# Kernel optimization log

Measured on AMD Instinct MI355X. Metric: run time of the kernel, lower is better.

Reference implementation:

```python
import jax, jax.numpy as jnp
import numpy as np

N, M, D, H, T = 8192, 8192, 64, 32, 8
KERNEL_SCALE = 1.0


def setup_inputs() -> dict:
    key = jax.random.key(0)
    ks = jax.random.split(key, 8)
    s1 = 1.0 / np.sqrt(D)
    s2 = 1.0 / np.sqrt(H)
    return {
        "X": jax.random.normal(ks[0], (N, D), jnp.float32),
        "Y": jax.random.normal(ks[1], (M, D), jnp.float32),
        "Y_target": jax.random.normal(ks[2], (M, T), jnp.float32),
        "W1": jax.random.normal(ks[3], (D, H), jnp.float32) * s1,
        "b1": jnp.zeros((H,), jnp.float32),
        "W2": jax.random.normal(ks[4], (H, H), jnp.float32) * s2,
        "b2": jnp.zeros((H,), jnp.float32),
        "W3": jax.random.normal(ks[5], (H, H), jnp.float32) * s2,
        "b3": jnp.zeros((H,), jnp.float32),
    }


def _mlp(x, W1, b1, W2, b2, W3, b3):
    h = jax.nn.relu(x @ W1 + b1)
    h = jax.nn.relu(h @ W2 + b2)
    return jax.nn.relu(h @ W3 + b3)


def reference(X, Y, Y_target, W1, b1, W2, b2, W3, b3):
    Xf = _mlp(X, W1, b1, W2, b2, W3, b3)  # [N, H]
    Yf = _mlp(Y, W1, b1, W2, b2, W3, b3)  # [M, H]
    sq = (
        jnp.sum(Xf * Xf, axis=1, keepdims=True)
        + jnp.sum(Yf * Yf, axis=1)[None, :]
        - 2.0 * (Xf @ Yf.T)
    )
    sq = jnp.maximum(sq, 0.0)  # guard tiny negatives from cancellation
    kernel = jnp.exp(-sq / (2.0 * KERNEL_SCALE**2))  # [N, M]
    weights = kernel / jnp.sum(kernel, axis=1, keepdims=True)
    return weights @ Y_target  # [N, T]
```

## Files before the change

kernel.cpp:

```cpp
#include <hip/hip_runtime.h>
#include <hip/hip_bf16.h>
#include <cstddef>

#define N_ROWS 8192
#define M_ROWS 8192
#define D_IN   64
#define H_DIM  32
#define T_OUT  8

#define NSPLIT   16
#define JSLICE   (M_ROWS / NSPLIT)
#define JTILE    32
#define NTILES   (JSLICE / JTILE)
#define LOG2E    1.4426950408889634f
#define NHALF_SC (-0.72134752044448169f)
#define PSTRIDE  34

typedef _Float16 half8  __attribute__((ext_vector_type(8)));
typedef __fp16   fp16x2 __attribute__((ext_vector_type(2)));
typedef float    f32x4  __attribute__((ext_vector_type(4)));
typedef float    f32x16 __attribute__((ext_vector_type(16)));

__device__ __forceinline__ half8 ld_h8(const _Float16* p) {
    return *(const half8*)p;
}

__global__ __launch_bounds__(256) void feat_kernel(
    const float* __restrict__ X, const float* __restrict__ Y,
    const float* __restrict__ W1, const float* __restrict__ b1,
    const float* __restrict__ W2, const float* __restrict__ b2,
    const float* __restrict__ W3, const float* __restrict__ b3,
    _Float16* __restrict__ fh, _Float16* __restrict__ fl,
    float* __restrict__ ns)
{
    __shared__ float xs [32 * 65];
    __shared__ float w1l[64 * 36];
    __shared__ float w2l[32 * 36];
    __shared__ float w3l[32 * 36];
    __shared__ float h1t[32 * 33];
    __shared__ float h2t[32 * 33];
    __shared__ float psums[8 * 32];
    __shared__ float bl[96];

    const int tid = threadIdx.x;
    const int rowbase = blockIdx.x * 32;
    const bool isX = rowbase < N_ROWS;
    const float* src = isX ? (X + (size_t)rowbase * D_IN)
                           : (Y + (size_t)(rowbase - N_ROWS) * D_IN);

    {
        const float4* g4 = (const float4*)src;
        int i0 = tid * 2;
        float4 v0 = g4[i0], v1 = g4[i0 + 1];
        int f0 = tid * 8;
        int r = f0 >> 6, c = f0 & 63;
        float* dst = xs + r * 65 + c;
        dst[0] = v0.x; dst[1] = v0.y; dst[2] = v0.z; dst[3] = v0.w;
        dst[4] = v1.x; dst[5] = v1.y; dst[6] = v1.z; dst[7] = v1.w;
    }
    {
        const float4* g4 = (const float4*)W1;
        int i0 = tid * 2;
        float4 v0 = g4[i0], v1 = g4[i0 + 1];
        int f0 = tid * 8;
        int r = f0 >> 5, c = f0 & 31;
        float* dst = w1l + r * 36 + c;
        ((float4*)dst)[0] = v0; ((float4*)dst)[1] = v1;
    }
    {
        int f0 = tid * 4;
        int r = f0 >> 5, c = f0 & 31;
        *(float4*)(w2l + r * 36 + c) = ((const float4*)W2)[tid];
        *(float4*)(w3l + r * 36 + c) = ((const float4*)W3)[tid];
    }
    if (tid < 32) { bl[tid] = b1[tid]; bl[32 + tid] = b2[tid]; bl[64 + tid] = b3[tid]; }
    __syncthreads();

    const int r  = tid & 31;
    const int c0 = (tid >> 5) * 4;

    float4 a1 = *(const float4*)(bl + c0);
    #pragma unroll
    for (int k = 0; k < 64; ++k) {
        float xv = xs[r * 65 + k];
        float4 w = *(const float4*)(w1l + k * 36 + c0);
        a1.x = fmaf(xv, w.x, a1.x);
        a1.y = fmaf(xv, w.y, a1.y);
        a1.z = fmaf(xv, w.z, a1.z);
        a1.w = fmaf(xv, w.w, a1.w);
    }
    h1t[(c0 + 0) * 33 + r] = fmaxf(a1.x, 0.f);
    h1t[(c0 + 1) * 33 + r] = fmaxf(a1.y, 0.f);
    h1t[(c0 + 2) * 33 + r] = fmaxf(a1.z, 0.f);
    h1t[(c0 + 3) * 33 + r] = fmaxf(a1.w, 0.f);
    __syncthreads();

    float4 a2 = *(const float4*)(bl + 32 + c0);
    #pragma unroll
    for (int k = 0; k < 32; ++k) {
        float xv = h1t[k * 33 + r];
        float4 w = *(const float4*)(w2l + k * 36 + c0);
        a2.x = fmaf(xv, w.x, a2.x);
        a2.y = fmaf(xv, w.y, a2.y);
        a2.z = fmaf(xv, w.z, a2.z);
        a2.w = fmaf(xv, w.w, a2.w);
    }
    h2t[(c0 + 0) * 33 + r] = fmaxf(a2.x, 0.f);
    h2t[(c0 + 1) * 33 + r] = fmaxf(a2.y, 0.f);
    h2t[(c0 + 2) * 33 + r] = fmaxf(a2.z, 0.f);
    h2t[(c0 + 3) * 33 + r] = fmaxf(a2.w, 0.f);
    __syncthreads();

    float4 a3 = *(const float4*)(bl + 64 + c0);
    #pragma unroll
    for (int k = 0; k < 32; ++k) {
        float xv = h2t[k * 33 + r];
        float4 w = *(const float4*)(w3l + k * 36 + c0);
        a3.x = fmaf(xv, w.x, a3.x);
        a3.y = fmaf(xv, w.y, a3.y);
        a3.z = fmaf(xv, w.z, a3.z);
        a3.w = fmaf(xv, w.w, a3.w);
    }
    float v0 = fmaxf(a3.x, 0.f), v1 = fmaxf(a3.y, 0.f);
    float v2 = fmaxf(a3.z, 0.f), v3 = fmaxf(a3.w, 0.f);

    float part = v0 * v0 + v1 * v1 + v2 * v2 + v3 * v3;
    psums[(tid >> 5) * 32 + r] = part;

    const float scale = isX ? LOG2E : 1.0f;
    union { _Float16 h[4]; uint2 u; } hh, ll;
    float sv0 = v0 * scale, sv1 = v1 * scale, sv2 = v2 * scale, sv3 = v3 * scale;
    hh.h[0] = (_Float16)sv0; hh.h[1] = (_Float16)sv1;
    hh.h[2] = (_Float16)sv2; hh.h[3] = (_Float16)sv3;
    ll.h[0] = (_Float16)(sv0 - (float)hh.h[0]);
    ll.h[1] = (_Float16)(sv1 - (float)hh.h[1]);
    ll.h[2] = (_Float16)(sv2 - (float)hh.h[2]);
    ll.h[3] = (_Float16)(sv3 - (float)hh.h[3]);
    const size_t fo = (size_t)(rowbase + r) * H_DIM + c0;
    *(uint2*)(fh + fo) = hh.u;
    *(uint2*)(fl + fo) = ll.u;

    __syncthreads();
    if (tid < 32) {
        float nrm = 0.f;
        #pragma unroll
        for (int g = 0; g < 8; ++g) nrm += psums[g * 32 + tid];
        ns[rowbase + tid] = NHALF_SC * nrm;
    }
}

__global__ __launch_bounds__(256) void ytt_kernel(
    const float* __restrict__ Yt,
    _Float16* __restrict__ yth, _Float16* __restrict__ ytl)
{
    const int c = blockIdx.x * 256 + threadIdx.x;
    #pragma unroll
    for (int t = 0; t < 16; ++t) {
        float v = (t < T_OUT) ? Yt[(size_t)c * T_OUT + t] : (t == 8 ? 1.0f : 0.0f);
        _Float16 hi = (_Float16)v;
        yth[(size_t)t * M_ROWS + c] = hi;
        ytl[(size_t)t * M_ROWS + c] = (_Float16)(v - (float)hi);
    }
}

__global__ __launch_bounds__(256, 4) void pair_kernel(
    const _Float16* __restrict__ fh, const _Float16* __restrict__ fl,
    const float* __restrict__ ns,
    const _Float16* __restrict__ yth, const _Float16* __restrict__ ytl,
    float* __restrict__ pout, float* __restrict__ psum)
{
    __shared__ unsigned int plds[4][32 * PSTRIDE];

    const int tid  = threadIdx.x;
    const int wave = tid >> 6;
    const int lane = tid & 63;
    const int n    = lane & 31;
    const int h    = lane >> 5;
    const int m16  = lane & 15;
    const int quad = lane >> 4;

    const int rowbase = blockIdx.x * 128 + wave * 32;
    const int s       = blockIdx.y;
    const int jstart  = s * JSLICE;

    unsigned int* pw = plds[wave];

    const _Float16* qp = fh + (size_t)(rowbase + n) * H_DIM + h * 8;
    const _Float16* qpl = fl + (size_t)(rowbase + n) * H_DIM + h * 8;
    half8 qh0 = ld_h8(qp);
    half8 qh1 = ld_h8(qp + 16);
    half8 ql0 = ld_h8(qpl);
    half8 ql1 = ld_h8(qpl + 16);

    float qv[16];
    #pragma unroll
    for (int r = 0; r < 16; ++r) {
        int rr = (r & 3) + 8 * (r >> 2) + 4 * h;
        qv[r] = ns[rowbase + rr];
    }

    f32x4 pv0 = {}; f32x4 pv1 = {};

    for (int jt = 0; jt < NTILES; ++jt) {
        const int jbase = jstart + jt * JTILE;

        const _Float16* kp  = fh + (size_t)(N_ROWS + jbase + n) * H_DIM + h * 8;
        const _Float16* kpl = fl + (size_t)(N_ROWS + jbase + n) * H_DIM + h * 8;
        half8 kh0 = ld_h8(kp);
        half8 kh1 = ld_h8(kp + 16);
        half8 kl0 = ld_h8(kpl);
        half8 kl1 = ld_h8(kpl + 16);
        const float ck = ns[N_ROWS + jbase + n];

        half8 yh = ld_h8(yth + (size_t)m16 * M_ROWS + jbase + quad * 8);
        half8 yl = ld_h8(ytl + (size_t)m16 * M_ROWS + jbase + quad * 8);

        f32x16 acc = {};
        acc = __builtin_amdgcn_mfma_f32_32x32x16_f16(qh0, kh0, acc, 0, 0, 0);
        acc = __builtin_amdgcn_mfma_f32_32x32x16_f16(qh1, kh1, acc, 0, 0, 0);
        acc = __builtin_amdgcn_mfma_f32_32x32x16_f16(qh0, kl0, acc, 0, 0, 0);
        acc = __builtin_amdgcn_mfma_f32_32x32x16_f16(qh1, kl1, acc, 0, 0, 0);
        acc = __builtin_amdgcn_mfma_f32_32x32x16_f16(ql0, kh0, acc, 0, 0, 0);
        acc = __builtin_amdgcn_mfma_f32_32x32x16_f16(ql1, kh1, acc, 0, 0, 0);

        #pragma unroll
        for (int r = 0; r < 16; ++r) {
            float t = fminf(acc[r] + (qv[r] + ck), 0.0f);
            float w = __builtin_amdgcn_exp2f(t);
            fp16x2 u = __builtin_amdgcn_cvt_pkrtz(w, w);
            float back = (float)u[0];
            fp16x2 d = __builtin_amdgcn_cvt_pkrtz(w, w - back);
            int rr = (r & 3) + 8 * (r >> 2) + 4 * h;
            pw[rr * PSTRIDE + n] = __builtin_bit_cast(unsigned int, d);
        }

        #pragma unroll
        for (int H = 0; H < 2; ++H) {
            const unsigned int* rp = pw + (H * 16 + m16) * PSTRIDE + quad * 8;
            uint2 e0 = *(const uint2*)(rp + 0);
            uint2 e1 = *(const uint2*)(rp + 2);
            uint2 e2 = *(const uint2*)(rp + 4);
            uint2 e3 = *(const uint2*)(rp + 6);
            union { unsigned int u[4]; half8 v; } ahi, alo;
            ahi.u[0] = __builtin_amdgcn_perm(e0.y, e0.x, 0x05040100u);
            ahi.u[1] = __builtin_amdgcn_perm(e1.y, e1.x, 0x05040100u);
            ahi.u[2] = __builtin_amdgcn_perm(e2.y, e2.x, 0x05040100u);
            ahi.u[3] = __builtin_amdgcn_perm(e3.y, e3.x, 0x05040100u);
            alo.u[0] = __builtin_amdgcn_perm(e0.y, e0.x, 0x07060302u);
            alo.u[1] = __builtin_amdgcn_perm(e1.y, e1.x, 0x07060302u);
            alo.u[2] = __builtin_amdgcn_perm(e2.y, e2.x, 0x07060302u);
            alo.u[3] = __builtin_amdgcn_perm(e3.y, e3.x, 0x07060302u);
            if (H == 0) {
                pv0 = __builtin_amdgcn_mfma_f32_16x16x32_f16(ahi.v, yh, pv0, 0, 0, 0);
                pv0 = __builtin_amdgcn_mfma_f32_16x16x32_f16(alo.v, yh, pv0, 0, 0, 0);
                pv0 = __builtin_amdgcn_mfma_f32_16x16x32_f16(ahi.v, yl, pv0, 0, 0, 0);
            } else {
                pv1 = __builtin_amdgcn_mfma_f32_16x16x32_f16(ahi.v, yh, pv1, 0, 0, 0);
                pv1 = __builtin_amdgcn_mfma_f32_16x16x32_f16(alo.v, yh, pv1, 0, 0, 0);
                pv1 = __builtin_amdgcn_mfma_f32_16x16x32_f16(ahi.v, yl, pv1, 0, 0, 0);
            }
        }
    }

    const int t = m16;
    if (t <= 8) {
        #pragma unroll
        for (int H = 0; H < 2; ++H) {
            #pragma unroll
            for (int r = 0; r < 4; ++r) {
                int row = rowbase + H * 16 + quad * 4 + r;
                float v = H ? pv1[r] : pv0[r];
                if (t < 8)
                    pout[((size_t)s * N_ROWS + row) * T_OUT + t] = v;
                else
                    psum[(size_t)s * N_ROWS + row] = v;
            }
        }
    }
}

__global__ __launch_bounds__(256) void reduce_kernel(
    const float* __restrict__ pout, const float* __restrict__ psum,
    float* __restrict__ out)
{
    const int id = blockIdx.x * 256 + threadIdx.x;
    const int i = id >> 3;
    float sv = 0.f, sw = 0.f;
    #pragma unroll
    for (int s = 0; s < NSPLIT; ++s) {
        sv += pout[(size_t)s * N_ROWS * T_OUT + id];
        sw += psum[(size_t)s * N_ROWS + i];
    }
    out[id] = sv / sw;
}

extern "C" void kernel_launch(void* const* d_in, const int* in_sizes, int n_in,
                              void* d_out, int out_size, void* d_ws, size_t ws_size,
                              hipStream_t stream)
{
    const float* X  = (const float*)d_in[0];
    const float* Y  = (const float*)d_in[1];
    const float* Yt = (const float*)d_in[2];
    const float* W1 = (const float*)d_in[3];
    const float* b1 = (const float*)d_in[4];
    const float* W2 = (const float*)d_in[5];
    const float* b2 = (const float*)d_in[6];
    const float* W3 = (const float*)d_in[7];
    const float* b3 = (const float*)d_in[8];
    float* out = (float*)d_out;

    char* ws = (char*)d_ws;
    const size_t n_feat = (size_t)(N_ROWS + M_ROWS) * H_DIM;
    _Float16* fh  = (_Float16*)ws;                 ws += n_feat * 2;
    _Float16* fl  = (_Float16*)ws;                 ws += n_feat * 2;
    float*    ns  = (float*)ws;                    ws += (N_ROWS + M_ROWS) * 4;
    _Float16* yth = (_Float16*)ws;                 ws += 16 * M_ROWS * 2;
    _Float16* ytl = (_Float16*)ws;                 ws += 16 * M_ROWS * 2;
    float*    pout = (float*)ws;                   ws += (size_t)NSPLIT * N_ROWS * T_OUT * 4;
    float*    psum = (float*)ws;

    feat_kernel<<<(N_ROWS + M_ROWS) / 32, 256, 0, stream>>>(
        X, Y, W1, b1, W2, b2, W3, b3, fh, fl, ns);
    ytt_kernel<<<M_ROWS / 256, 256, 0, stream>>>(Yt, yth, ytl);

    dim3 grid2(N_ROWS / 128, NSPLIT);
    pair_kernel<<<grid2, 256, 0, stream>>>(fh, fl, ns, yth, ytl, pout, psum);

    reduce_kernel<<<(N_ROWS * T_OUT) / 256, 256, 0, stream>>>(pout, psum, out);
}
```

Measured before the change: 116.7 us.

## Fold norm terms into augmented features and feed P directly to MFMA without LDS

Each feature vector is extended from 32 to 48 fp16 columns, with two extra columns carrying the scaled squared norm and a 1, so the pairwise bias comes out of the QK MFMA directly. This removes the per-element norm add and the ns loads. The MFMA operand order is swapped so the exp2 result already sits in the register layout the 32x32x8 P·V MFMA expects, which removes the LDS round trip, the perm shuffles and the shared buffer. Y_target is pre-tiled into that layout by ytt_kernel. In exchange it issues more QK MFMAs per tile (9 instead of 6) and reads wider feature rows, and putting the norms in fp16 hi/lo pairs may cost some accuracy.

```diff
diff --git a/kernel.cpp b/kernel.cpp
--- a/kernel.cpp
+++ b/kernel.cpp
@@ -7,6 +7,7 @@
 #define D_IN   64
 #define H_DIM  32
 #define T_OUT  8
+#define FDIM   48
 
 #define NSPLIT   16
 #define JSLICE   (M_ROWS / NSPLIT)
@@ -14,11 +15,10 @@
 #define NTILES   (JSLICE / JTILE)
 #define LOG2E    1.4426950408889634f
 #define NHALF_SC (-0.72134752044448169f)
-#define PSTRIDE  34
 
 typedef _Float16 half8  __attribute__((ext_vector_type(8)));
+typedef _Float16 half4v __attribute__((ext_vector_type(4)));
 typedef __fp16   fp16x2 __attribute__((ext_vector_type(2)));
-typedef float    f32x4  __attribute__((ext_vector_type(4)));
 typedef float    f32x16 __attribute__((ext_vector_type(16)));
 
 __device__ __forceinline__ half8 ld_h8(const _Float16* p) {
@@ -30,8 +30,7 @@
     const float* __restrict__ W1, const float* __restrict__ b1,
     const float* __restrict__ W2, const float* __restrict__ b2,
     const float* __restrict__ W3, const float* __restrict__ b3,
-    _Float16* __restrict__ fh, _Float16* __restrict__ fl,
-    float* __restrict__ ns)
+    _Float16* __restrict__ fh, _Float16* __restrict__ fl)
 {
     __shared__ float xs [32 * 65];
     __shared__ float w1l[64 * 36];
@@ -124,8 +123,7 @@
     float v0 = fmaxf(a3.x, 0.f), v1 = fmaxf(a3.y, 0.f);
     float v2 = fmaxf(a3.z, 0.f), v3 = fmaxf(a3.w, 0.f);
 
-    float part = v0 * v0 + v1 * v1 + v2 * v2 + v3 * v3;
-    psums[(tid >> 5) * 32 + r] = part;
+    psums[(tid >> 5) * 32 + r] = v0 * v0 + v1 * v1 + v2 * v2 + v3 * v3;
 
     const float scale = isX ? LOG2E : 1.0f;
     union { _Float16 h[4]; uint2 u; } hh, ll;
@@ -136,7 +134,7 @@
     ll.h[1] = (_Float16)(sv1 - (float)hh.h[1]);
     ll.h[2] = (_Float16)(sv2 - (float)hh.h[2]);
     ll.h[3] = (_Float16)(sv3 - (float)hh.h[3]);
-    const size_t fo = (size_t)(rowbase + r) * H_DIM + c0;
+    const size_t fo = (size_t)(rowbase + r) * FDIM + c0;
     *(uint2*)(fh + fo) = hh.u;
     *(uint2*)(fl + fo) = ll.u;
 
@@ -145,136 +143,135 @@
         float nrm = 0.f;
         #pragma unroll
         for (int g = 0; g < 8; ++g) nrm += psums[g * 32 + tid];
-        ns[rowbase + tid] = NHALF_SC * nrm;
+        float qn = NHALF_SC * nrm;
+        float d32 = isX ? qn : 1.0f;
+        float d33 = isX ? 1.0f : qn;
+        union { _Float16 h[16]; uint4 q[2]; } eh, el;
+        #pragma unroll
+        for (int i = 0; i < 16; ++i) { eh.h[i] = (_Float16)0.f; el.h[i] = (_Float16)0.f; }
+        _Float16 h32 = (_Float16)d32, h33 = (_Float16)d33;
+        eh.h[0] = h32; eh.h[1] = h33;
+        el.h[0] = (_Float16)(d32 - (float)h32);
+        el.h[1] = (_Float16)(d33 - (float)h33);
+        const size_t eo = (size_t)(rowbase + tid) * FDIM + 32;
+        *(uint4*)(fh + eo) = eh.q[0]; *(uint4*)(fh + eo + 8) = eh.q[1];
+        *(uint4*)(fl + eo) = el.q[0]; *(uint4*)(fl + eo + 8) = el.q[1];
     }
 }
 
 __global__ __launch_bounds__(256) void ytt_kernel(
     const float* __restrict__ Yt,
-    _Float16* __restrict__ yth, _Float16* __restrict__ ytl)
-{
-    const int c = blockIdx.x * 256 + threadIdx.x;
-    #pragma unroll
-    for (int t = 0; t < 16; ++t) {
-        float v = (t < T_OUT) ? Yt[(size_t)c * T_OUT + t] : (t == 8 ? 1.0f : 0.0f);
+    _Float16* __restrict__ yfh, _Float16* __restrict__ yfl)
+{
+    const int idx = blockIdx.x * 256 + threadIdx.x;
+    const int lane = idx & 63;
+    const int jtg  = idx >> 6;
+    const int g    = jtg & 3;
+    const int jt   = jtg >> 2;
+    const int t    = lane & 31;
+    const int h    = lane >> 5;
+    const int j    = jt * 32 + g * 8 + h * 4;
+    union { _Float16 hh[4]; uint2 u; } H, L;
+    #pragma unroll
+    for (int i = 0; i < 4; ++i) {
+        float v = (t < T_OUT) ? Yt[(size_t)(j + i) * T_OUT + t]
+                              : (t == 8 ? 1.0f : 0.0f);
         _Float16 hi = (_Float16)v;
-        yth[(size_t)t * M_ROWS + c] = hi;
-        ytl[(size_t)t * M_ROWS + c] = (_Float16)(v - (float)hi);
-    }
+        H.hh[i] = hi;
+        L.hh[i] = (_Float16)(v - (float)hi);
+    }
+    *(uint2*)(yfh + (size_t)idx * 4) = H.u;
+    *(uint2*)(yfl + (size_t)idx * 4) = L.u;
 }
 
 __global__ __launch_bounds__(256, 4) void pair_kernel(
     const _Float16* __restrict__ fh, const _Float16* __restrict__ fl,
-    const float* __restrict__ ns,
-    const _Float16* __restrict__ yth, const _Float16* __restrict__ ytl,
+    const _Float16* __restrict__ yfh, const _Float16* __restrict__ yfl,
     float* __restrict__ pout, float* __restrict__ psum)
 {
-    __shared__ unsigned int plds[4][32 * PSTRIDE];
-
     const int tid  = threadIdx.x;
     const int wave = tid >> 6;
     const int lane = tid & 63;
     const int n    = lane & 31;
     const int h    = lane >> 5;
-    const int m16  = lane & 15;
-    const int quad = lane >> 4;
 
     const int rowbase = blockIdx.x * 128 + wave * 32;
     const int s       = blockIdx.y;
     const int jstart  = s * JSLICE;
 
-    unsigned int* pw = plds[wave];
-
-    const _Float16* qp = fh + (size_t)(rowbase + n) * H_DIM + h * 8;
-    const _Float16* qpl = fl + (size_t)(rowbase + n) * H_DIM + h * 8;
-    half8 qh0 = ld_h8(qp);
-    half8 qh1 = ld_h8(qp + 16);
-    half8 ql0 = ld_h8(qpl);
-    half8 ql1 = ld_h8(qpl + 16);
-
-    float qv[16];
-    #pragma unroll
-    for (int r = 0; r < 16; ++r) {
-        int rr = (r & 3) + 8 * (r >> 2) + 4 * h;
-        qv[r] = ns[rowbase + rr];
-    }
-
-    f32x4 pv0 = {}; f32x4 pv1 = {};
+    const _Float16* qb  = fh + (size_t)(rowbase + n) * FDIM + h * 8;
+    const _Float16* qbl = fl + (size_t)(rowbase + n) * FDIM + h * 8;
+    half8 qh0 = ld_h8(qb);        half8 qh1 = ld_h8(qb + 16);
+    half8 qh2 = ld_h8(qb + 32);
+    half8 ql0 = ld_h8(qbl);       half8 ql1 = ld_h8(qbl + 16);
+    half8 ql2 = ld_h8(qbl + 32);
+
+    f32x16 o = {};
 
     for (int jt = 0; jt < NTILES; ++jt) {
         const int jbase = jstart + jt * JTILE;
 
-        const _Float16* kp  = fh + (size_t)(N_ROWS + jbase + n) * H_DIM + h * 8;
-        const _Float16* kpl = fl + (size_t)(N_ROWS + jbase + n) * H_DIM + h * 8;
-        half8 kh0 = ld_h8(kp);
-        half8 kh1 = ld_h8(kp + 16);
-        half8 kl0 = ld_h8(kpl);
-        half8 kl1 = ld_h8(kpl + 16);
-        const float ck = ns[N_ROWS + jbase + n];
-
-        half8 yh = ld_h8(yth + (size_t)m16 * M_ROWS + jbase + quad * 8);
-        half8 yl = ld_h8(ytl + (size_t)m16 * M_ROWS + jbase + quad * 8);
+        const _Float16* ka  = fh + (size_t)(N_ROWS + jbase + n) * FDIM + h * 8;
+        const _Float16* kal = fl + (size_t)(N_ROWS + jbase + n) * FDIM + h * 8;
+        half8 kh0 = ld_h8(ka);        half8 kh1 = ld_h8(ka + 16);
+        half8 kh2 = ld_h8(ka + 32);
+        half8 kl0 = ld_h8(kal);       half8 kl1 = ld_h8(kal + 16);
+        half8 kl2 = ld_h8(kal + 32);
 
         f32x16 acc = {};
-        acc = __builtin_amdgcn_mfma_f32_32x32x16_f16(qh0, kh0, acc, 0, 0, 0);
-        acc = __builtin_amdgcn_mfma_f32_32x32x16_f16(qh1, kh1, acc, 0, 0, 0);
-        acc = __builtin_amdgcn_mfma_f32_32x32x16_f16(qh0, kl0, acc, 0, 0, 0);
-        acc = __builtin_amdgcn_mfma_f32_32x32x16_f16(qh1, kl1, acc, 0, 0, 0);
-        acc = __builtin_amdgcn_mfma_f32_32x32x16_f16(ql0, kh0, acc, 0, 0, 0);
-        acc = __builtin_amdgcn_mfma_f32_32x32x16_f16(ql1, kh1, acc, 0, 0, 0);
-
+        acc = __builtin_amdgcn_mfma_f32_32x32x16_f16(kh0, qh0, acc, 0, 0, 0);
+        acc = __builtin_amdgcn_mfma_f32_32x32x16_f16(kh1, qh1, acc, 0, 0, 0);
+        acc = __builtin_amdgcn_mfma_f32_32x32x16_f16(kh2, qh2, acc, 0, 0, 0);
+        acc = __builtin_amdgcn_mfma_f32_32x32x16_f16(kh0, ql0, acc, 0, 0, 0);
+        acc = __builtin_amdgcn_mfma_f32_32x32x16_f16(kh1, ql1, acc, 0, 0, 0);
+        acc = __builtin_amdgcn_mfma_f32_32x32x16_f16(kh2, ql2, acc, 0, 0, 0);
+        acc = __builtin_amdgcn_mfma_f32_32x32x16_f16(kl0, qh0, acc, 0, 0, 0);
+        acc = __builtin_amdgcn_mfma_f32_32x32x16_f16(kl1, qh1, acc, 0, 0, 0);
+        acc = __builtin_amdgcn_mfma_f32_32x32x16_f16(kl2, qh2, acc, 0, 0, 0);
+
+        half4v phi[4], plo[4];
+        #pragma unroll
+        for (int g = 0; g < 4; ++g) {
+            float w0 = __builtin_amdgcn_exp2f(fminf(acc[4*g+0], 0.f));
+            float w1 = __builtin_amdgcn_exp2f(fminf(acc[4*g+1], 0.f));
+            float w2 = __builtin_amdgcn_exp2f(fminf(acc[4*g+2], 0.f));
+            float w3 = __builtin_amdgcn_exp2f(fminf(acc[4*g+3], 0.f));
+            fp16x2 p01 = __builtin_amdgcn_cvt_pkrtz(w0, w1);
+            fp16x2 p23 = __builtin_amdgcn_cvt_pkrtz(w2, w3);
+            fp16x2 l01 = __builtin_amdgcn_cvt_pkrtz(w0 - (float)p01[0],
+                                                    w1 - (float)p01[1]);
+            fp16x2 l23 = __builtin_amdgcn_cvt_pkrtz(w2 - (float)p23[0],
+                                                    w3 - (float)p23[1]);
+            union { unsigned int u[2]; half4v v; } ph, pl;
+            ph.u[0] = __builtin_bit_cast(unsigned int, p01);
+            ph.u[1] = __builtin_bit_cast(unsigned int, p23);
+            pl.u[0] = __builtin_bit_cast(unsigned int, l01);
+            pl.u[1] = __builtin_bit_cast(unsigned int, l23);
+            phi[g] = ph.v; plo[g] = pl.v;
+        }
+
+        const size_t yb = ((size_t)((s * NTILES + jt) * 4) * 64 + lane) * 4;
+        #pragma unroll
+        for (int g = 0; g < 4; ++g) {
+            half4v bh = *(const half4v*)(yfh + yb + (size_t)g * 256);
+            half4v bl = *(const half4v*)(yfl + yb + (size_t)g * 256);
+            o = __builtin_amdgcn_mfma_f32_32x32x8f16(phi[g], bh, o, 0, 0, 0);
+            o = __builtin_amdgcn_mfma_f32_32x32x8f16(plo[g], bh, o, 0, 0, 0);
+            o = __builtin_amdgcn_mfma_f32_32x32x8f16(phi[g], bl, o, 0, 0, 0);
+        }
+    }
+
+    const int t = n;
+    if (t <= 8) {
         #pragma unroll
         for (int r = 0; r < 16; ++r) {
-            float t = fminf(acc[r] + (qv[r] + ck), 0.0f);
-            float w = __builtin_amdgcn_exp2f(t);
-            fp16x2 u = __builtin_amdgcn_cvt_pkrtz(w, w);
-            float back = (float)u[0];
-            fp16x2 d = __builtin_amdgcn_cvt_pkrtz(w, w - back);
-            int rr = (r & 3) + 8 * (r >> 2) + 4 * h;
-            pw[rr * PSTRIDE + n] = __builtin_bit_cast(unsigned int, d);
-        }
-
-        #pragma unroll
-        for (int H = 0; H < 2; ++H) {
-            const unsigned int* rp = pw + (H * 16 + m16) * PSTRIDE + quad * 8;
-            uint2 e0 = *(const uint2*)(rp + 0);
-            uint2 e1 = *(const uint2*)(rp + 2);
-            uint2 e2 = *(const uint2*)(rp + 4);
-            uint2 e3 = *(const uint2*)(rp + 6);
-            union { unsigned int u[4]; half8 v; } ahi, alo;
-            ahi.u[0] = __builtin_amdgcn_perm(e0.y, e0.x, 0x05040100u);
-            ahi.u[1] = __builtin_amdgcn_perm(e1.y, e1.x, 0x05040100u);
-            ahi.u[2] = __builtin_amdgcn_perm(e2.y, e2.x, 0x05040100u);
-            ahi.u[3] = __builtin_amdgcn_perm(e3.y, e3.x, 0x05040100u);
-            alo.u[0] = __builtin_amdgcn_perm(e0.y, e0.x, 0x07060302u);
-            alo.u[1] = __builtin_amdgcn_perm(e1.y, e1.x, 0x07060302u);
-            alo.u[2] = __builtin_amdgcn_perm(e2.y, e2.x, 0x07060302u);
-            alo.u[3] = __builtin_amdgcn_perm(e3.y, e3.x, 0x07060302u);
-            if (H == 0) {
-                pv0 = __builtin_amdgcn_mfma_f32_16x16x32_f16(ahi.v, yh, pv0, 0, 0, 0);
-                pv0 = __builtin_amdgcn_mfma_f32_16x16x32_f16(alo.v, yh, pv0, 0, 0, 0);
-                pv0 = __builtin_amdgcn_mfma_f32_16x16x32_f16(ahi.v, yl, pv0, 0, 0, 0);
-            } else {
-                pv1 = __builtin_amdgcn_mfma_f32_16x16x32_f16(ahi.v, yh, pv1, 0, 0, 0);
-                pv1 = __builtin_amdgcn_mfma_f32_16x16x32_f16(alo.v, yh, pv1, 0, 0, 0);
-                pv1 = __builtin_amdgcn_mfma_f32_16x16x32_f16(ahi.v, yl, pv1, 0, 0, 0);
-            }
-        }
-    }
-
-    const int t = m16;
-    if (t <= 8) {
-        #pragma unroll
-        for (int H = 0; H < 2; ++H) {
-            #pragma unroll
-            for (int r = 0; r < 4; ++r) {
-                int row = rowbase + H * 16 + quad * 4 + r;
-                float v = H ? pv1[r] : pv0[r];
-                if (t < 8)
-                    pout[((size_t)s * N_ROWS + row) * T_OUT + t] = v;
-                else
-                    psum[(size_t)s * N_ROWS + row] = v;
-            }
+            int i = (r & 3) + 8 * (r >> 2) + 4 * h;
+            int row = rowbase + i;
+            float v = o[r];
+            if (t < 8)
+                pout[((size_t)s * N_ROWS + row) * T_OUT + t] = v;
+            else
+                psum[(size_t)s * N_ROWS + row] = v;
         }
     }
 }
@@ -310,21 +307,21 @@
     float* out = (float*)d_out;
 
     char* ws = (char*)d_ws;
-    const size_t n_feat = (size_t)(N_ROWS + M_ROWS) * H_DIM;
-    _Float16* fh  = (_Float16*)ws;                 ws += n_feat * 2;
-    _Float16* fl  = (_Float16*)ws;                 ws += n_feat * 2;
-    float*    ns  = (float*)ws;                    ws += (N_ROWS + M_ROWS) * 4;
-    _Float16* yth = (_Float16*)ws;                 ws += 16 * M_ROWS * 2;
-    _Float16* ytl = (_Float16*)ws;                 ws += 16 * M_ROWS * 2;
-    float*    pout = (float*)ws;                   ws += (size_t)NSPLIT * N_ROWS * T_OUT * 4;
+    const size_t n_feat = (size_t)(N_ROWS + M_ROWS) * FDIM;
+    _Float16* fh  = (_Float16*)ws;   ws += n_feat * 2;
+    _Float16* fl  = (_Float16*)ws;   ws += n_feat * 2;
+    const size_t n_yf = (size_t)(M_ROWS / JTILE) * 4 * 64 * 4;
+    _Float16* yfh = (_Float16*)ws;   ws += n_yf * 2;
+    _Float16* yfl = (_Float16*)ws;   ws += n_yf * 2;
+    float*    pout = (float*)ws;     ws += (size_t)NSPLIT * N_ROWS * T_OUT * 4;
     float*    psum = (float*)ws;
 
     feat_kernel<<<(N_ROWS + M_ROWS) / 32, 256, 0, stream>>>(
-        X, Y, W1, b1, W2, b2, W3, b3, fh, fl, ns);
-    ytt_kernel<<<M_ROWS / 256, 256, 0, stream>>>(Yt, yth, ytl);
+        X, Y, W1, b1, W2, b2, W3, b3, fh, fl);
+    ytt_kernel<<<(M_ROWS / JTILE) * 4 * 64 / 256, 256, 0, stream>>>(Yt, yfh, yfl);
 
     dim3 grid2(N_ROWS / 128, NSPLIT);
-    pair_kernel<<<grid2, 256, 0, stream>>>(fh, fl, ns, yth, ytl, pout, psum);
+    pair_kernel<<<grid2, 256, 0, stream>>>(fh, fl, yfh, yfl, pout, psum);
 
     reduce_kernel<<<(N_ROWS * T_OUT) / 256, 256, 0, stream>>>(pout, psum, out);
 }
```

Result: slower. 122.5 us (+5.0%).
